# Kernel optimization log

Hardware: AMD Instinct MI355X
Metric: run time of the kernel (lower is better)

Reference implementation:

```python
import jax, jax.numpy as jnp
import numpy as np

S, N, D, F, L = 16, 64, 1270, 150, 8  # sentences, entities, emb dim, ffnn_size, num_labels


def _xavier(key, shape):
    lim = np.sqrt(6.0 / (shape[0] + shape[1])).astype(np.float32)
    return jax.random.uniform(key, shape, jnp.float32, -lim, lim)


def setup_inputs() -> dict:
    key = jax.random.key(0)
    ks = jax.random.split(key, 8)
    entity_emb = jax.random.normal(ks[0], (S, N, D), jnp.float32)
    entity_scores = jax.random.normal(ks[1], (S, N), jnp.float32)
    rel_labels = jax.random.randint(ks[2], (S, N, N), 0, L)
    num_predicted_entities = jax.random.randint(ks[3], (S,), 0, N)
    # Linear params stored [in, out] (y = x @ W + b), transpose of torch layout.
    W_in = _xavier(ks[4], (3 * D, F))
    b_in = jnp.zeros((F,), jnp.float32)
    W_h = _xavier(ks[5], (F, F))
    b_h = jnp.zeros((F,), jnp.float32)
    W_out = _xavier(ks[6], (F, L - 1))
    b_out = jnp.zeros((L - 1,), jnp.float32)
    return {
        "entity_emb": entity_emb,
        "entity_scores": entity_scores,
        "W_in": W_in, "b_in": b_in,
        "W_h": W_h, "b_h": b_h,
        "W_out": W_out, "b_out": b_out,
        "rel_labels": rel_labels,
        "num_predicted_entities": num_predicted_entities,
    }


def reference(entity_emb, entity_scores, W_in, b_in, W_h, b_h, W_out, b_out,
              rel_labels, num_predicted_entities):
    s, n, d = entity_emb.shape
    # pair_emb = concat([e1_tiled, e2_tiled, e1*e2]) @ W_in  ==  split-weight fused form
    # (avoids materializing the [S,N,N,3D] tensor; same math).
    W1, W2, W3 = W_in[:d], W_in[d:2 * d], W_in[2 * d:]
    h = (jnp.einsum('sid,df->sif', entity_emb, W1)[:, :, None, :]
         + jnp.einsum('sjd,df->sjf', entity_emb, W2)[:, None, :, :]
         + jnp.einsum('sid,sjd,df->sijf', entity_emb, entity_emb, W3)
         + b_in)  # [S,N,N,F]
    # NOTE: original applies two more Linear layers with NO nonlinearity between them.
    h = h @ W_h + b_h
    scores = h @ W_out + b_out  # [S,N,N,L-1]
    # dropout is identity at inference (reference baseline)
    rel = scores + entity_scores[:, :, None, None] + entity_scores[:, None, :, None]
    dummy = jnp.zeros((s, n, n, 1), rel.dtype)
    rel_scores = jnp.concatenate([dummy, rel], axis=3)  # [S,N,N,L]
    # per-element cross entropy (reduction='none'), then pair mask, then sum
    logp = jax.nn.log_softmax(rel_scores, axis=-1)
    ce = -jnp.take_along_axis(logp, rel_labels[..., None], axis=-1)[..., 0]  # [S,N,N]
    ent_mask = jnp.arange(n)[None, :] < num_predicted_entities[:, None]  # [S,N]
    pair_mask = ent_mask[:, :, None] & ent_mask[:, None, :]  # [S,N,N]
    loss = jnp.sum(jnp.where(pair_mask, ce, jnp.zeros((), ce.dtype)))
    return rel_scores, loss
```

## Files before the change

kernel.cpp:

```cpp
#include <hip/hip_runtime.h>
#include <hip/hip_bf16.h>
#include <stdint.h>

typedef __attribute__((ext_vector_type(8))) short bf16x8;
typedef __attribute__((ext_vector_type(16))) float f32x16;

#define S_ 16
#define N_ 64
#define D_ 1270
#define F_ 150
#define KP_ 1280
#define FP_ 160
#define NKT 80
#define LOSS_OFF (S_*N_*N_*8)

#define HSTR 172

__device__ inline short f2b(float x) {
    union { float f; uint32_t u; } v; v.f = x;
    uint32_t r = (v.u + 0x7fffu + ((v.u >> 16) & 1u)) >> 16;
    return (short)r;
}
__device__ inline bf16x8 as_bf16x8(uint4 u) {
    union { uint4 a; bf16x8 b; } c; c.a = u; return c.b;
}

__global__ void k_pack(const float* __restrict__ emb, const float* __restrict__ win,
                       const float* __restrict__ wh, const float* __restrict__ wout,
                       short* __restrict__ eapk, short* __restrict__ w3pk,
                       short* __restrict__ w12pk, short* __restrict__ whpk,
                       short* __restrict__ wopk) {
    int t = blockIdx.x * 256 + threadIdx.x;
    const int TOT_EA = S_ * NKT * 2 * 64;
    const int NW3 = NKT * 5 * 64, NW12 = NKT * 10 * 64, NWH = 10 * 5 * 64, NWO = 10 * 64;
    if (t < TOT_EA) {
        int l  = t & 63;
        int mt = (t >> 6) & 1;
        int kt = (t >> 7) % NKT;
        int s  = t / (NKT * 2 * 64);
        int i  = (l & 31) + mt * 32;
        int k0 = kt * 16 + (l >> 5) * 8;
        const float* src = emb + (size_t)(s * N_ + i) * D_;
        bf16x8 pk;
        if (k0 + 8 <= D_) {
            float2 v0 = *(const float2*)(src + k0);
            float2 v1 = *(const float2*)(src + k0 + 2);
            float2 v2 = *(const float2*)(src + k0 + 4);
            float2 v3 = *(const float2*)(src + k0 + 6);
            pk[0]=f2b(v0.x); pk[1]=f2b(v0.y); pk[2]=f2b(v1.x); pk[3]=f2b(v1.y);
            pk[4]=f2b(v2.x); pk[5]=f2b(v2.y); pk[6]=f2b(v3.x); pk[7]=f2b(v3.y);
        } else {
            #pragma unroll
            for (int u = 0; u < 8; ++u) {
                int k = k0 + u;
                pk[u] = (k < D_) ? f2b(src[k]) : (short)0;
            }
        }
        *(bf16x8*)(eapk + (size_t)t * 8) = pk;
        return;
    }
    int t0 = t - TOT_EA;
    if (t0 < NW3) {
        int l = t0 & 63, nt = (t0 >> 6) % 5, kt = t0 / 320;
        int k0 = kt * 16 + (l >> 5) * 8, f = (l & 31) + nt * 32;
        bf16x8 pk;
        #pragma unroll
        for (int u = 0; u < 8; ++u) {
            int k = k0 + u;
            pk[u] = (k < D_ && f < F_) ? f2b(win[((size_t)(2 * D_) + k) * F_ + f]) : (short)0;
        }
        *(bf16x8*)(w3pk + (size_t)t0 * 8) = pk;
    } else if (t0 < NW3 + NW12) {
        int t2 = t0 - NW3;
        int l = t2 & 63, nt = (t2 >> 6) % 10, kt = t2 / 640;
        int k0 = kt * 16 + (l >> 5) * 8, c = (l & 31) + nt * 32;
        bf16x8 pk;
        #pragma unroll
        for (int u = 0; u < 8; ++u) {
            int k = k0 + u;
            float val = 0.f;
            if (k < D_) {
                if (c < FP_) { if (c < F_) val = win[(size_t)k * F_ + c]; }
                else { int f = c - FP_; if (f < F_) val = win[((size_t)D_ + k) * F_ + f]; }
            }
            pk[u] = f2b(val);
        }
        *(bf16x8*)(w12pk + (size_t)t2 * 8) = pk;
    } else if (t0 < NW3 + NW12 + NWH) {
        int t3 = t0 - NW3 - NW12;
        int l = t3 & 63, nt = (t3 >> 6) % 5, kt = t3 / 320;
        int k0 = kt * 16 + (l >> 5) * 8, f = (l & 31) + nt * 32;
        bf16x8 pk;
        #pragma unroll
        for (int u = 0; u < 8; ++u) {
            int k = k0 + u;
            pk[u] = (k < F_ && f < F_) ? f2b(wh[(size_t)k * F_ + f]) : (short)0;
        }
        *(bf16x8*)(whpk + (size_t)t3 * 8) = pk;
    } else if (t0 < NW3 + NW12 + NWH + NWO) {
        int t4 = t0 - NW3 - NW12 - NWH;
        int l = t4 & 63, kt = t4 >> 6;
        int k0 = kt * 16 + (l >> 5) * 8, f = l & 31;
        bf16x8 pk;
        #pragma unroll
        for (int u = 0; u < 8; ++u) {
            int k = k0 + u;
            pk[u] = (k < F_ && f < 7) ? f2b(wout[k * 7 + f]) : (short)0;
        }
        *(bf16x8*)(wopk + (size_t)t4 * 8) = pk;
    }
}

__global__ __launch_bounds__(128) void k_p12(const short* __restrict__ eapk,
                                             const short* __restrict__ w12pk,
                                             const float* __restrict__ bin,
                                             float* __restrict__ p1, float* __restrict__ p2) {
    __shared__ float red[16][64];
    int bid = blockIdx.x;
    int s = bid / 20, rr = bid % 20;
    int nt = rr >> 1, mt = rr & 1;
    int lane = threadIdx.x & 63, ks = threadIdx.x >> 6;
    f32x16 acc;
    #pragma unroll
    for (int r = 0; r < 16; ++r) acc[r] = 0.f;
    const size_t abase = (size_t)s * NKT * 2 * 64 * 8;
    #pragma unroll 8
    for (int kt = ks * 40; kt < ks * 40 + 40; ++kt) {
        bf16x8 a = *(const bf16x8*)(eapk + abase + ((size_t)kt * 2 + mt) * 64 * 8 + (size_t)lane * 8);
        bf16x8 b = *(const bf16x8*)(w12pk + ((size_t)(kt * 10 + nt) * 64 + lane) * 8);
        acc = __builtin_amdgcn_mfma_f32_32x32x16_bf16(a, b, acc, 0, 0, 0);
    }
    if (ks == 1) {
        #pragma unroll
        for (int r = 0; r < 16; ++r) red[r][lane] = acc[r];
    }
    __syncthreads();
    if (ks == 0) {
        int c = (lane & 31) + nt * 32;
        #pragma unroll
        for (int r = 0; r < 16; ++r) {
            float v = acc[r] + red[r][lane];
            int i = (r & 3) + 8 * (r >> 2) + 4 * (lane >> 5) + mt * 32;
            if (c < FP_) {
                p1[(size_t)(s * N_ + i) * FP_ + c] = v;
            } else {
                int f = c - FP_;
                float bv = (f < F_) ? bin[f] : 0.f;
                p2[(size_t)(s * N_ + i) * FP_ + f] = v + bv;
            }
        }
    }
}

template<int NB>
__device__ __forceinline__ void run_gemm1(const char* ea, const char* w3,
                                          const float* ej0, const float* ej1,
                                          f32x16 (&acc)[2][3]) {
    uint4 euA, euB;
    uint4 bfA[3], bfB[3];

    auto fetch = [&](int kt, uint4& eu, uint4 (&bfv)[3]) {
        eu = *(const uint4*)(ea + (size_t)kt * 2048);
        #pragma unroll
        for (int nb = 0; nb < NB; ++nb)
            bfv[nb] = *(const uint4*)(w3 + (size_t)kt * 5120 + nb * 1024);
    };
    auto step = [&](int kt, const uint4& eu, const uint4 (&bfv)[3]) {
        float4 a0 = *(const float4*)(ej0 + kt * 16);
        float4 a1 = *(const float4*)(ej0 + kt * 16 + 4);
        float4 b0 = *(const float4*)(ej1 + kt * 16);
        float4 b1 = *(const float4*)(ej1 + kt * 16 + 4);
        float ev0[8] = {a0.x,a0.y,a0.z,a0.w,a1.x,a1.y,a1.z,a1.w};
        float ev1[8] = {b0.x,b0.y,b0.z,b0.w,b1.x,b1.y,b1.z,b1.w};
        uint32_t ew[4] = {eu.x, eu.y, eu.z, eu.w};
        union { uint32_t u[4]; bf16x8 v; } av0, av1;
        #pragma unroll
        for (int p = 0; p < 4; ++p) {
            float elo = __uint_as_float(ew[p] << 16);
            float ehi = __uint_as_float(ew[p] & 0xffff0000u);
            float f00 = elo * ev0[2*p], f01 = ehi * ev0[2*p+1];
            float f10 = elo * ev1[2*p], f11 = ehi * ev1[2*p+1];
            uint32_t p0, p1v;
            asm("v_cvt_pk_bf16_f32 %0, %1, %2" : "=v"(p0)  : "v"(f00), "v"(f01));
            asm("v_cvt_pk_bf16_f32 %0, %1, %2" : "=v"(p1v) : "v"(f10), "v"(f11));
            av0.u[p] = p0; av1.u[p] = p1v;
        }
        #pragma unroll
        for (int nb = 0; nb < NB; ++nb) {
            bf16x8 bb = as_bf16x8(bfv[nb]);
            acc[0][nb] = __builtin_amdgcn_mfma_f32_32x32x16_bf16(av0.v, bb, acc[0][nb], 0, 0, 0);
            acc[1][nb] = __builtin_amdgcn_mfma_f32_32x32x16_bf16(av1.v, bb, acc[1][nb], 0, 0, 0);
        }
    };

    fetch(0, euA, bfA);
    fetch(1, euB, bfB);
    #pragma unroll 1
    for (int kt = 0; kt < NKT; kt += 2) {
        step(kt, euA, bfA);
        if (kt + 2 < NKT) fetch(kt + 2, euA, bfA);
        step(kt + 1, euB, bfB);
        if (kt + 3 < NKT) fetch(kt + 3, euB, bfB);
    }
}

template<int NB, int NT0>
__device__ __forceinline__ void write_h(const f32x16 (&acc)[2][3], short* hB,
                                        const float* p1s, const float* p2r0,
                                        const float* p2r1, int lane, int mt) {
    #pragma unroll
    for (int nb = 0; nb < NB; ++nb) {
        const int f = (lane & 31) + (NT0 + nb) * 32;
        float p1v[16];
        #pragma unroll
        for (int r = 0; r < 16; ++r) {
            int i = (r & 3) + 8 * (r >> 2) + 4 * (lane >> 5) + mt * 32;
            p1v[r] = p1s[(size_t)i * FP_ + f];
        }
        const float p20 = p2r0[f], p21 = p2r1[f];
        #pragma unroll
        for (int r = 0; r < 16; ++r) {
            int i = (r & 3) + 8 * (r >> 2) + 4 * (lane >> 5) + mt * 32;
            hB[i * HSTR + f]             = f2b(acc[0][nb][r] + p1v[r] + p20);
            hB[64 * HSTR + i * HSTR + f] = f2b(acc[1][nb][r] + p1v[r] + p21);
        }
    }
}

__global__ __launch_bounds__(256, 1) void k_main(
    const float* __restrict__ emb, const float* __restrict__ esc,
    const short* __restrict__ eapk, const short* __restrict__ w3pk,
    const short* __restrict__ whpk, const short* __restrict__ wopk,
    const float* __restrict__ p1g, const float* __restrict__ p2g,
    const float* __restrict__ bhv, const float* __restrict__ bout,
    const int* __restrict__ labels, const int* __restrict__ nump,
    float* __restrict__ out) {

    __shared__ char lds[48128];
    float* sbuf = (float*)lds;
    float* ejB  = (float*)(lds + 4096);
    short* hB   = (short*)(lds + 4096);

    const int tid = threadIdx.x, lane = tid & 63, w = tid >> 6;
    const int mt = w & 1, nh = w >> 1;
    const int bid = blockIdx.x, s = bid >> 5, j0 = (bid & 31) * 2;

    for (int idx = tid; idx < 2 * KP_; idx += 256) {
        int jr = idx / KP_, k = idx - jr * KP_;
        ejB[idx] = (k < D_) ? emb[(size_t)(s * N_ + j0 + jr) * D_ + k] : 0.f;
    }
    __syncthreads();

    f32x16 acc[2][3];
    #pragma unroll
    for (int jl = 0; jl < 2; ++jl)
        #pragma unroll
        for (int nb = 0; nb < 3; ++nb)
            #pragma unroll
            for (int r = 0; r < 16; ++r) acc[jl][nb][r] = 0.f;

    {
        const char* ea = (const char*)eapk + (size_t)s * 163840 + mt * 1024 + lane * 16;
        const char* w3 = (const char*)w3pk + (nh ? 3 : 0) * 1024 + lane * 16;
        const float* ej0 = ejB + ((lane >> 5) << 3);
        const float* ej1 = ej0 + KP_;
        if (nh == 0) run_gemm1<3>(ea, w3, ej0, ej1, acc);
        else         run_gemm1<2>(ea, w3, ej0, ej1, acc);
    }
    __syncthreads();

    {
        const float* p1s = p1g + (size_t)(s * N_) * FP_;
        const float* p2r0 = p2g + (size_t)(s * N_ + j0) * FP_;
        const float* p2r1 = p2r0 + FP_;
        if (nh == 0) write_h<3, 0>(acc, hB, p1s, p2r0, p2r1, lane, mt);
        else         write_h<2, 3>(acc, hB, p1s, p2r0, p2r1, lane, mt);
    }
    __syncthreads();

    f32x16 acc2[5];
    #pragma unroll
    for (int c = 0; c < 5; ++c)
        #pragma unroll
        for (int r = 0; r < 16; ++r) acc2[c][r] = 0.f;
    #pragma unroll 1
    for (int kt = 0; kt < 10; ++kt) {
        #pragma unroll
        for (int c = 0; c < 5; ++c) {
            int t = w + 4 * c;
            int jl2 = t / 10, tt = t % 10;
            int mt2 = tt / 5, nt2 = tt % 5;
            const short* ap = hB + jl2 * (64 * HSTR) + ((lane & 31) + mt2 * 32) * HSTR
                            + kt * 16 + ((lane >> 5) << 3);
            short4 alo = *(const short4*)ap;
            short4 ahi = *(const short4*)(ap + 4);
            union { short sh[8]; bf16x8 v; } av;
            av.sh[0] = alo.x; av.sh[1] = alo.y; av.sh[2] = alo.z; av.sh[3] = alo.w;
            av.sh[4] = ahi.x; av.sh[5] = ahi.y; av.sh[6] = ahi.z; av.sh[7] = ahi.w;
            bf16x8 b = *(const bf16x8*)(whpk + ((size_t)(kt * 5 + nt2) * 64 + lane) * 8);
            acc2[c] = __builtin_amdgcn_mfma_f32_32x32x16_bf16(av.v, b, acc2[c], 0, 0, 0);
        }
    }
    __syncthreads();

    #pragma unroll
    for (int c = 0; c < 5; ++c) {
        int t = w + 4 * c;
        int jl2 = t / 10, tt = t % 10;
        int mt2 = tt / 5, nt2 = tt % 5;
        int f = (lane & 31) + nt2 * 32;
        float bhf = (f < F_) ? bhv[f] : 0.f;
        #pragma unroll
        for (int r = 0; r < 16; ++r) {
            int i = (r & 3) + 8 * (r >> 2) + 4 * (lane >> 5) + mt2 * 32;
            short hv = (f < F_) ? f2b(acc2[c][r] + bhf) : (short)0;
            hB[jl2 * (64 * HSTR) + i * HSTR + f] = hv;
        }
    }
    __syncthreads();

    {
        int jl3 = w >> 1, mt3 = w & 1;
        f32x16 acc3;
        #pragma unroll
        for (int r = 0; r < 16; ++r) acc3[r] = 0.f;
        #pragma unroll 1
        for (int kt = 0; kt < 10; ++kt) {
            const short* ap = hB + jl3 * (64 * HSTR) + ((lane & 31) + mt3 * 32) * HSTR
                            + kt * 16 + ((lane >> 5) << 3);
            short4 alo = *(const short4*)ap;
            short4 ahi = *(const short4*)(ap + 4);
            union { short sh[8]; bf16x8 v; } av;
            av.sh[0] = alo.x; av.sh[1] = alo.y; av.sh[2] = alo.z; av.sh[3] = alo.w;
            av.sh[4] = ahi.x; av.sh[5] = ahi.y; av.sh[6] = ahi.z; av.sh[7] = ahi.w;
            bf16x8 b = *(const bf16x8*)(wopk + ((size_t)(kt * 64) + lane) * 8);
            acc3 = __builtin_amdgcn_mfma_f32_32x32x16_bf16(av.v, b, acc3, 0, 0, 0);
        }
        int c3 = lane & 31;
        if (c3 < 7) {
            float bo = bout[c3];
            #pragma unroll
            for (int r = 0; r < 16; ++r) {
                int i = (r & 3) + 8 * (r >> 2) + 4 * (lane >> 5) + mt3 * 32;
                sbuf[jl3 * 512 + i * 8 + c3] = acc3[r] + bo;
            }
        }
    }
    __syncthreads();

    if (tid < 128) {
        int jl = tid >> 6;
        int i = tid & 63;
        int j = j0 + jl;
        const float esi = esc[s * N_ + i];
        const float esj = esc[s * N_ + j];
        float rr[8];
        rr[0] = 0.f;
        #pragma unroll
        for (int l = 1; l < 8; ++l) rr[l] = sbuf[jl * 512 + i * 8 + (l - 1)] + esi + esj;

        float4* op = (float4*)(out + ((size_t)(s * N_ + i) * N_ + j) * 8);
        op[0] = make_float4(rr[0], rr[1], rr[2], rr[3]);
        op[1] = make_float4(rr[4], rr[5], rr[6], rr[7]);

        float m = rr[0];
        #pragma unroll
        for (int l = 1; l < 8; ++l) m = fmaxf(m, rr[l]);
        float sum = 0.f;
        #pragma unroll
        for (int l = 0; l < 8; ++l) sum += expf(rr[l] - m);
        const float lse = m + logf(sum);

        const int lab = labels[(s * N_ + i) * N_ + j];
        float ce = lse - rr[lab];
        const int np = nump[s];
        float v = (i < np && j < np) ? ce : 0.f;
        #pragma unroll
        for (int off = 32; off; off >>= 1) v += __shfl_down(v, off);
        if ((tid & 63) == 0) atomicAdd(out + LOSS_OFF, v);
    }
}

extern "C" void kernel_launch(void* const* d_in, const int* in_sizes, int n_in,
                              void* d_out, int out_size, void* d_ws, size_t ws_size,
                              hipStream_t stream) {
    const float* emb    = (const float*)d_in[0];
    const float* esc    = (const float*)d_in[1];
    const float* Win    = (const float*)d_in[2];
    const float* bin    = (const float*)d_in[3];
    const float* Wh     = (const float*)d_in[4];
    const float* bh     = (const float*)d_in[5];
    const float* Wout   = (const float*)d_in[6];
    const float* bout   = (const float*)d_in[7];
    const int*   labels = (const int*)d_in[8];
    const int*   nump   = (const int*)d_in[9];
    float* out = (float*)d_out;

    char* ws = (char*)d_ws;
    short* eapk  = (short*)(ws);
    short* w3pk  = (short*)(ws + 2621440);
    short* w12pk = (short*)(ws + 3031040);
    short* whpk  = (short*)(ws + 3850240);
    short* wopk  = (short*)(ws + 3901440);
    float* p1    = (float*)(ws + 3911680);
    float* p2    = (float*)(ws + 4567040);

    hipMemsetAsync(out + LOSS_OFF, 0, sizeof(float), stream);

    const int TOT_EA = S_ * NKT * 2 * 64;
    const int NW = NKT * 5 * 64 + NKT * 10 * 64 + 10 * 5 * 64 + 10 * 64;
    k_pack<<<(TOT_EA + NW + 255) / 256, 256, 0, stream>>>(emb, Win, Wh, Wout,
                                                          eapk, w3pk, w12pk, whpk, wopk);
    k_p12<<<320, 128, 0, stream>>>(eapk, w12pk, bin, p1, p2);
    k_main<<<S_ * 32, 256, 0, stream>>>(emb, esc, eapk, w3pk, whpk, wopk, p1, p2,
                                        bh, bout, labels, nump, out);
}
```

Before: 93.92 us.

## Process one j per block in main kernel and split p12 K-loop four ways

The main kernel now handles a single j column per block instead of two, doubling the grid to S*N blocks and halving LDS and accumulator registers. This raises occupancy and parallelism, but each block reloads the shared eapk and W3 tiles, so W3 traffic doubles. The GEMM1 prefetch depth goes from 2 to 4 stages. k_p12 uses 4 waves splitting the K loop in quarters, reduced through LDS, to shorten its serial MFMA chain.

```diff
diff --git a/kernel.cpp b/kernel.cpp
--- a/kernel.cpp
+++ b/kernel.cpp
@@ -111,11 +111,11 @@
     }
 }
 
-__global__ __launch_bounds__(128) void k_p12(const short* __restrict__ eapk,
+__global__ __launch_bounds__(256) void k_p12(const short* __restrict__ eapk,
                                              const short* __restrict__ w12pk,
                                              const float* __restrict__ bin,
                                              float* __restrict__ p1, float* __restrict__ p2) {
-    __shared__ float red[16][64];
+    __shared__ float red[3][16][64];
     int bid = blockIdx.x;
     int s = bid / 20, rr = bid % 20;
     int nt = rr >> 1, mt = rr & 1;
@@ -124,22 +124,22 @@
     #pragma unroll
     for (int r = 0; r < 16; ++r) acc[r] = 0.f;
     const size_t abase = (size_t)s * NKT * 2 * 64 * 8;
-    #pragma unroll 8
-    for (int kt = ks * 40; kt < ks * 40 + 40; ++kt) {
+    #pragma unroll 4
+    for (int kt = ks * 20; kt < ks * 20 + 20; ++kt) {
         bf16x8 a = *(const bf16x8*)(eapk + abase + ((size_t)kt * 2 + mt) * 64 * 8 + (size_t)lane * 8);
         bf16x8 b = *(const bf16x8*)(w12pk + ((size_t)(kt * 10 + nt) * 64 + lane) * 8);
         acc = __builtin_amdgcn_mfma_f32_32x32x16_bf16(a, b, acc, 0, 0, 0);
     }
-    if (ks == 1) {
-        #pragma unroll
-        for (int r = 0; r < 16; ++r) red[r][lane] = acc[r];
+    if (ks > 0) {
+        #pragma unroll
+        for (int r = 0; r < 16; ++r) red[ks - 1][r][lane] = acc[r];
     }
     __syncthreads();
     if (ks == 0) {
         int c = (lane & 31) + nt * 32;
         #pragma unroll
         for (int r = 0; r < 16; ++r) {
-            float v = acc[r] + red[r][lane];
+            float v = acc[r] + red[0][r][lane] + red[1][r][lane] + red[2][r][lane];
             int i = (r & 3) + 8 * (r >> 2) + 4 * (lane >> 5) + mt * 32;
             if (c < FP_) {
                 p1[(size_t)(s * N_ + i) * FP_ + c] = v;
@@ -153,76 +153,69 @@
 }
 
 template<int NB>
+__device__ __forceinline__ void fetch1(const char* ea, const char* w3, int kt,
+                                       uint4& eu, uint4 (&bfv)[3]) {
+    eu = *(const uint4*)(ea + (size_t)kt * 2048);
+    #pragma unroll
+    for (int nb = 0; nb < NB; ++nb)
+        bfv[nb] = *(const uint4*)(w3 + (size_t)kt * 5120 + nb * 1024);
+}
+
+template<int NB>
+__device__ __forceinline__ void step1(int kt, const uint4& eu, const uint4 (&bfv)[3],
+                                      const float* ej0, f32x16 (&acc)[3]) {
+    float4 a0 = *(const float4*)(ej0 + kt * 16);
+    float4 a1 = *(const float4*)(ej0 + kt * 16 + 4);
+    float ev[8] = {a0.x,a0.y,a0.z,a0.w,a1.x,a1.y,a1.z,a1.w};
+    uint32_t ew[4] = {eu.x, eu.y, eu.z, eu.w};
+    union { uint32_t u[4]; bf16x8 v; } av;
+    #pragma unroll
+    for (int p = 0; p < 4; ++p) {
+        float flo = __uint_as_float(ew[p] << 16) * ev[2 * p];
+        float fhi = __uint_as_float(ew[p] & 0xffff0000u) * ev[2 * p + 1];
+        uint32_t pk;
+        asm("v_cvt_pk_bf16_f32 %0, %1, %2" : "=v"(pk) : "v"(flo), "v"(fhi));
+        av.u[p] = pk;
+    }
+    #pragma unroll
+    for (int nb = 0; nb < NB; ++nb)
+        acc[nb] = __builtin_amdgcn_mfma_f32_32x32x16_bf16(av.v, as_bf16x8(bfv[nb]), acc[nb], 0, 0, 0);
+}
+
+template<int NB>
 __device__ __forceinline__ void run_gemm1(const char* ea, const char* w3,
-                                          const float* ej0, const float* ej1,
-                                          f32x16 (&acc)[2][3]) {
-    uint4 euA, euB;
-    uint4 bfA[3], bfB[3];
-
-    auto fetch = [&](int kt, uint4& eu, uint4 (&bfv)[3]) {
-        eu = *(const uint4*)(ea + (size_t)kt * 2048);
-        #pragma unroll
-        for (int nb = 0; nb < NB; ++nb)
-            bfv[nb] = *(const uint4*)(w3 + (size_t)kt * 5120 + nb * 1024);
-    };
-    auto step = [&](int kt, const uint4& eu, const uint4 (&bfv)[3]) {
-        float4 a0 = *(const float4*)(ej0 + kt * 16);
-        float4 a1 = *(const float4*)(ej0 + kt * 16 + 4);
-        float4 b0 = *(const float4*)(ej1 + kt * 16);
-        float4 b1 = *(const float4*)(ej1 + kt * 16 + 4);
-        float ev0[8] = {a0.x,a0.y,a0.z,a0.w,a1.x,a1.y,a1.z,a1.w};
-        float ev1[8] = {b0.x,b0.y,b0.z,b0.w,b1.x,b1.y,b1.z,b1.w};
-        uint32_t ew[4] = {eu.x, eu.y, eu.z, eu.w};
-        union { uint32_t u[4]; bf16x8 v; } av0, av1;
-        #pragma unroll
-        for (int p = 0; p < 4; ++p) {
-            float elo = __uint_as_float(ew[p] << 16);
-            float ehi = __uint_as_float(ew[p] & 0xffff0000u);
-            float f00 = elo * ev0[2*p], f01 = ehi * ev0[2*p+1];
-            float f10 = elo * ev1[2*p], f11 = ehi * ev1[2*p+1];
-            uint32_t p0, p1v;
-            asm("v_cvt_pk_bf16_f32 %0, %1, %2" : "=v"(p0)  : "v"(f00), "v"(f01));
-            asm("v_cvt_pk_bf16_f32 %0, %1, %2" : "=v"(p1v) : "v"(f10), "v"(f11));
-            av0.u[p] = p0; av1.u[p] = p1v;
-        }
-        #pragma unroll
-        for (int nb = 0; nb < NB; ++nb) {
-            bf16x8 bb = as_bf16x8(bfv[nb]);
-            acc[0][nb] = __builtin_amdgcn_mfma_f32_32x32x16_bf16(av0.v, bb, acc[0][nb], 0, 0, 0);
-            acc[1][nb] = __builtin_amdgcn_mfma_f32_32x32x16_bf16(av1.v, bb, acc[1][nb], 0, 0, 0);
-        }
-    };
-
-    fetch(0, euA, bfA);
-    fetch(1, euB, bfB);
+                                          const float* ej0, f32x16 (&acc)[3]) {
+    uint4 euA, euB, euC, euD;
+    uint4 bfA[3], bfB[3], bfC[3], bfD[3];
+    fetch1<NB>(ea, w3, 0, euA, bfA);
+    fetch1<NB>(ea, w3, 1, euB, bfB);
+    fetch1<NB>(ea, w3, 2, euC, bfC);
+    fetch1<NB>(ea, w3, 3, euD, bfD);
     #pragma unroll 1
-    for (int kt = 0; kt < NKT; kt += 2) {
-        step(kt, euA, bfA);
-        if (kt + 2 < NKT) fetch(kt + 2, euA, bfA);
-        step(kt + 1, euB, bfB);
-        if (kt + 3 < NKT) fetch(kt + 3, euB, bfB);
+    for (int kt = 0; kt < NKT; kt += 4) {
+        step1<NB>(kt + 0, euA, bfA, ej0, acc);
+        if (kt + 4 < NKT) fetch1<NB>(ea, w3, kt + 4, euA, bfA);
+        step1<NB>(kt + 1, euB, bfB, ej0, acc);
+        if (kt + 5 < NKT) fetch1<NB>(ea, w3, kt + 5, euB, bfB);
+        step1<NB>(kt + 2, euC, bfC, ej0, acc);
+        if (kt + 6 < NKT) fetch1<NB>(ea, w3, kt + 6, euC, bfC);
+        step1<NB>(kt + 3, euD, bfD, ej0, acc);
+        if (kt + 7 < NKT) fetch1<NB>(ea, w3, kt + 7, euD, bfD);
     }
 }
 
 template<int NB, int NT0>
-__device__ __forceinline__ void write_h(const f32x16 (&acc)[2][3], short* hB,
-                                        const float* p1s, const float* p2r0,
-                                        const float* p2r1, int lane, int mt) {
+__device__ __forceinline__ void write_h1(const f32x16 (&acc)[3], short* hB,
+                                         const float* p1s, const float* p2r,
+                                         int lane, int mt) {
     #pragma unroll
     for (int nb = 0; nb < NB; ++nb) {
         const int f = (lane & 31) + (NT0 + nb) * 32;
-        float p1v[16];
+        const float p2v = p2r[f];
         #pragma unroll
         for (int r = 0; r < 16; ++r) {
             int i = (r & 3) + 8 * (r >> 2) + 4 * (lane >> 5) + mt * 32;
-            p1v[r] = p1s[(size_t)i * FP_ + f];
-        }
-        const float p20 = p2r0[f], p21 = p2r1[f];
-        #pragma unroll
-        for (int r = 0; r < 16; ++r) {
-            int i = (r & 3) + 8 * (r >> 2) + 4 * (lane >> 5) + mt * 32;
-            hB[i * HSTR + f]             = f2b(acc[0][nb][r] + p1v[r] + p20);
-            hB[64 * HSTR + i * HSTR + f] = f2b(acc[1][nb][r] + p1v[r] + p21);
+            hB[i * HSTR + f] = f2b(acc[nb][r] + p1s[(size_t)i * FP_ + f] + p2v);
         }
     }
 }
@@ -236,62 +229,54 @@
     const int* __restrict__ labels, const int* __restrict__ nump,
     float* __restrict__ out) {
 
-    __shared__ char lds[48128];
+    __shared__ char lds[24064];
     float* sbuf = (float*)lds;
-    float* ejB  = (float*)(lds + 4096);
-    short* hB   = (short*)(lds + 4096);
+    float* ejB  = (float*)(lds + 2048);
+    short* hB   = (short*)(lds + 2048);
 
     const int tid = threadIdx.x, lane = tid & 63, w = tid >> 6;
     const int mt = w & 1, nh = w >> 1;
-    const int bid = blockIdx.x, s = bid >> 5, j0 = (bid & 31) * 2;
-
-    for (int idx = tid; idx < 2 * KP_; idx += 256) {
-        int jr = idx / KP_, k = idx - jr * KP_;
-        ejB[idx] = (k < D_) ? emb[(size_t)(s * N_ + j0 + jr) * D_ + k] : 0.f;
-    }
-    __syncthreads();
-
-    f32x16 acc[2][3];
-    #pragma unroll
-    for (int jl = 0; jl < 2; ++jl)
-        #pragma unroll
-        for (int nb = 0; nb < 3; ++nb)
-            #pragma unroll
-            for (int r = 0; r < 16; ++r) acc[jl][nb][r] = 0.f;
-
+    const int bid = blockIdx.x, s = bid >> 6, j = bid & 63;
+
+    for (int idx = tid; idx < KP_; idx += 256)
+        ejB[idx] = (idx < D_) ? emb[(size_t)(s * N_ + j) * D_ + idx] : 0.f;
+    __syncthreads();
+
+    f32x16 acc[3];
+    #pragma unroll
+    for (int nb = 0; nb < 3; ++nb)
+        #pragma unroll
+        for (int r = 0; r < 16; ++r) acc[nb][r] = 0.f;
     {
         const char* ea = (const char*)eapk + (size_t)s * 163840 + mt * 1024 + lane * 16;
         const char* w3 = (const char*)w3pk + (nh ? 3 : 0) * 1024 + lane * 16;
         const float* ej0 = ejB + ((lane >> 5) << 3);
-        const float* ej1 = ej0 + KP_;
-        if (nh == 0) run_gemm1<3>(ea, w3, ej0, ej1, acc);
-        else         run_gemm1<2>(ea, w3, ej0, ej1, acc);
+        if (nh == 0) run_gemm1<3>(ea, w3, ej0, acc);
+        else         run_gemm1<2>(ea, w3, ej0, acc);
     }
     __syncthreads();
 
     {
         const float* p1s = p1g + (size_t)(s * N_) * FP_;
-        const float* p2r0 = p2g + (size_t)(s * N_ + j0) * FP_;
-        const float* p2r1 = p2r0 + FP_;
-        if (nh == 0) write_h<3, 0>(acc, hB, p1s, p2r0, p2r1, lane, mt);
-        else         write_h<2, 3>(acc, hB, p1s, p2r0, p2r1, lane, mt);
-    }
-    __syncthreads();
-
-    f32x16 acc2[5];
-    #pragma unroll
-    for (int c = 0; c < 5; ++c)
+        const float* p2r = p2g + (size_t)(s * N_ + j) * FP_;
+        if (nh == 0) write_h1<3, 0>(acc, hB, p1s, p2r, lane, mt);
+        else         write_h1<2, 3>(acc, hB, p1s, p2r, lane, mt);
+    }
+    __syncthreads();
+
+    f32x16 acc2[3];
+    #pragma unroll
+    for (int c = 0; c < 3; ++c)
         #pragma unroll
         for (int r = 0; r < 16; ++r) acc2[c][r] = 0.f;
     #pragma unroll 1
     for (int kt = 0; kt < 10; ++kt) {
         #pragma unroll
-        for (int c = 0; c < 5; ++c) {
+        for (int c = 0; c < 3; ++c) {
             int t = w + 4 * c;
-            int jl2 = t / 10, tt = t % 10;
-            int mt2 = tt / 5, nt2 = tt % 5;
-            const short* ap = hB + jl2 * (64 * HSTR) + ((lane & 31) + mt2 * 32) * HSTR
-                            + kt * 16 + ((lane >> 5) << 3);
+            if (t >= 10) break;
+            int mt2 = t / 5, nt2 = t % 5;
+            const short* ap = hB + ((lane & 31) + mt2 * 32) * HSTR + kt * 16 + ((lane >> 5) << 3);
             short4 alo = *(const short4*)ap;
             short4 ahi = *(const short4*)(ap + 4);
             union { short sh[8]; bf16x8 v; } av;
@@ -304,30 +289,29 @@
     __syncthreads();
 
     #pragma unroll
-    for (int c = 0; c < 5; ++c) {
+    for (int c = 0; c < 3; ++c) {
         int t = w + 4 * c;
-        int jl2 = t / 10, tt = t % 10;
-        int mt2 = tt / 5, nt2 = tt % 5;
+        if (t >= 10) break;
+        int mt2 = t / 5, nt2 = t % 5;
         int f = (lane & 31) + nt2 * 32;
         float bhf = (f < F_) ? bhv[f] : 0.f;
         #pragma unroll
         for (int r = 0; r < 16; ++r) {
             int i = (r & 3) + 8 * (r >> 2) + 4 * (lane >> 5) + mt2 * 32;
             short hv = (f < F_) ? f2b(acc2[c][r] + bhf) : (short)0;
-            hB[jl2 * (64 * HSTR) + i * HSTR + f] = hv;
-        }
-    }
-    __syncthreads();
-
-    {
-        int jl3 = w >> 1, mt3 = w & 1;
+            hB[i * HSTR + f] = hv;
+        }
+    }
+    __syncthreads();
+
+    if (w < 2) {
+        int mt3 = w;
         f32x16 acc3;
         #pragma unroll
         for (int r = 0; r < 16; ++r) acc3[r] = 0.f;
         #pragma unroll 1
         for (int kt = 0; kt < 10; ++kt) {
-            const short* ap = hB + jl3 * (64 * HSTR) + ((lane & 31) + mt3 * 32) * HSTR
-                            + kt * 16 + ((lane >> 5) << 3);
+            const short* ap = hB + ((lane & 31) + mt3 * 32) * HSTR + kt * 16 + ((lane >> 5) << 3);
             short4 alo = *(const short4*)ap;
             short4 ahi = *(const short4*)(ap + 4);
             union { short sh[8]; bf16x8 v; } av;
@@ -342,22 +326,20 @@
             #pragma unroll
             for (int r = 0; r < 16; ++r) {
                 int i = (r & 3) + 8 * (r >> 2) + 4 * (lane >> 5) + mt3 * 32;
-                sbuf[jl3 * 512 + i * 8 + c3] = acc3[r] + bo;
+                sbuf[i * 8 + c3] = acc3[r] + bo;
             }
         }
     }
     __syncthreads();
 
-    if (tid < 128) {
-        int jl = tid >> 6;
-        int i = tid & 63;
-        int j = j0 + jl;
+    if (tid < 64) {
+        int i = tid;
         const float esi = esc[s * N_ + i];
         const float esj = esc[s * N_ + j];
         float rr[8];
         rr[0] = 0.f;
         #pragma unroll
-        for (int l = 1; l < 8; ++l) rr[l] = sbuf[jl * 512 + i * 8 + (l - 1)] + esi + esj;
+        for (int l = 1; l < 8; ++l) rr[l] = sbuf[i * 8 + (l - 1)] + esi + esj;
 
         float4* op = (float4*)(out + ((size_t)(s * N_ + i) * N_ + j) * 8);
         op[0] = make_float4(rr[0], rr[1], rr[2], rr[3]);
@@ -377,7 +359,7 @@
         float v = (i < np && j < np) ? ce : 0.f;
         #pragma unroll
         for (int off = 32; off; off >>= 1) v += __shfl_down(v, off);
-        if ((tid & 63) == 0) atomicAdd(out + LOSS_OFF, v);
+        if (tid == 0) atomicAdd(out + LOSS_OFF, v);
     }
 }
 
@@ -411,7 +393,7 @@
     const int NW = NKT * 5 * 64 + NKT * 10 * 64 + 10 * 5 * 64 + 10 * 64;
     k_pack<<<(TOT_EA + NW + 255) / 256, 256, 0, stream>>>(emb, Win, Wh, Wout,
                                                           eapk, w3pk, w12pk, whpk, wopk);
-    k_p12<<<320, 128, 0, stream>>>(eapk, w12pk, bin, p1, p2);
-    k_main<<<S_ * 32, 256, 0, stream>>>(emb, esc, eapk, w3pk, whpk, wopk, p1, p2,
+    k_p12<<<320, 256, 0, stream>>>(eapk, w12pk, bin, p1, p2);
+    k_main<<<S_ * N_, 256, 0, stream>>>(emb, esc, eapk, w3pk, whpk, wopk, p1, p2,
                                         bh, bout, labels, nump, out);
 }
```

Result: slower. 102.7 us (+9.3%).
